# Performance work log

Hardware: AMD Instinct MI355X
Metric: run time of the kernel (lower is better)

The kernel has to match this reference:

```python
import jax, jax.numpy as jnp
import numpy as np

GRID_SIZE = 5
SPLINE_ORDER = 3


def b_splines(x):
    """Cox-de Boor B-spline bases. x: [N, in] -> [N, in, GRID_SIZE+SPLINE_ORDER]."""
    k = SPLINE_ORDER
    h = 2.0 / GRID_SIZE  # grid range [-1, 1]
    grid = jnp.arange(-k, GRID_SIZE + k + 1, dtype=x.dtype) * h - 1.0  # [G+2k+1]
    xe = x[..., None]  # [N, in, 1]
    b = ((xe >= grid[:-1]) & (xe < grid[1:])).astype(x.dtype)
    for j in range(1, k + 1):
        b = ((xe - grid[:-(j + 1)]) / (grid[j:-1] - grid[:-(j + 1)]) * b[..., :-1]
             + (grid[j + 1:] - xe) / (grid[j + 1:] - grid[1:-j]) * b[..., 1:])
    return b  # [N, in, G+k]


def kan_linear(x, base_w, spline_w):
    """efficient-KAN KANLinear: silu base branch + spline branch.
    x: [N, in], base_w: [out, in], spline_w: [out, in, G+k] -> [N, out]."""
    base = jnp.einsum('ni,oi->no', jax.nn.silu(x), base_w)
    spline = jnp.einsum('nig,oig->no', b_splines(x), spline_w)
    return base + spline


def setup_inputs() -> dict:
    key = jax.random.key(0)
    ks = jax.random.split(key, 8)
    C, R, G = 128, 8, GRID_SIZE + SPLINE_ORDER  # in_channels, reduced, n_bases
    B, H, W, D = 2, 64, 64, 64
    s = 0.1  # keep spline weights in a sane init range
    return {
        'x': jax.random.normal(ks[0], (B, C, H, W, D), dtype=jnp.float32),
        'ck1_base': jax.random.normal(ks[1], (R, C), dtype=jnp.float32) * s,
        'ck1_spline': jax.random.normal(ks[2], (R, C, G), dtype=jnp.float32) * s,
        'ck2_base': jax.random.normal(ks[3], (C, R), dtype=jnp.float32) * s,
        'ck2_spline': jax.random.normal(ks[4], (C, R, G), dtype=jnp.float32) * s,
        'conv_w': jax.random.normal(ks[5], (C,), dtype=jnp.float32) * 0.1,
        'sk_base': jax.random.normal(ks[6], (1, 1), dtype=jnp.float32),
        'sk_spline': jax.random.normal(ks[7], (1, 1, G), dtype=jnp.float32),
    }


def reference(x, ck1_base, ck1_spline, ck2_base, ck2_spline, conv_w, sk_base, sk_spline):
    B, C, H, W, D = x.shape
    # channel attention: avg/max pool -> KAN -> ReLU -> KAN, shared weights
    y_avg = jnp.mean(x, axis=(2, 3, 4))  # [B, C]
    y_max = jnp.max(x, axis=(2, 3, 4))   # [B, C]

    def channel_mlp(y):
        h1 = jax.nn.relu(kan_linear(y, ck1_base, ck1_spline))
        return kan_linear(h1, ck2_base, ck2_spline)

    channel_att = jax.nn.sigmoid(channel_mlp(y_avg) + channel_mlp(y_max))
    x_channel = x * channel_att[:, :, None, None, None]

    # spatial attention: 1x1x1 conv (C->1, no bias) then per-voxel 1->1 KAN
    y_spatial = jnp.einsum('bchwd,c->bhwd', x_channel, conv_w)
    y_flat = y_spatial.reshape(-1, 1)  # [B*H*W*D, 1]
    spatial_att = jax.nn.sigmoid(kan_linear(y_flat, sk_base, sk_spline))
    spatial_att = spatial_att.reshape(B, 1, H, W, D)
    return x_channel * spatial_att
```

## Files before the change

### kernel.cpp

```cpp
#include <hip/hip_runtime.h>
#include <math.h>

#define HWD 262144
#define C_CH 128
#define B_N 2
#define VT 128

typedef float f4 __attribute__((ext_vector_type(4)));

__device__ __forceinline__ float sigmoidf_(float v) {
    return 1.0f / (1.0f + expf(-v));
}

__device__ __forceinline__ void bspline8(float x, float* bs) {
    float g[12];
#pragma unroll
    for (int i = 0; i < 12; ++i) g[i] = (float)(i - 3) * 0.4f - 1.0f;
    float b[11];
#pragma unroll
    for (int t = 0; t < 11; ++t) b[t] = (x >= g[t] && x < g[t + 1]) ? 1.0f : 0.0f;
#pragma unroll
    for (int j = 1; j <= 3; ++j) {
#pragma unroll
        for (int t = 0; t + j < 11; ++t) {
            b[t] = (x - g[t]) / (g[t + j] - g[t]) * b[t]
                 + (g[t + j + 1] - x) / (g[t + j + 1] - g[t + 1]) * b[t + 1];
        }
    }
#pragma unroll
    for (int t = 0; t < 8; ++t) bs[t] = b[t];
}

__global__ __launch_bounds__(1024) void k1_pool(const float* __restrict__ x,
                                                float* __restrict__ ws) {
    int bid = blockIdx.x;
    const float4* xp = (const float4*)(x + (size_t)bid * HWD);
    int tid = threadIdx.x;
    float s = 0.0f, m = -INFINITY;
#pragma unroll 4
    for (int i = 0; i < 64; ++i) {
        float4 v = xp[(size_t)i * 1024 + tid];
        s += (v.x + v.y) + (v.z + v.w);
        m = fmaxf(m, fmaxf(fmaxf(v.x, v.y), fmaxf(v.z, v.w)));
    }
#pragma unroll
    for (int off = 32; off > 0; off >>= 1) {
        s += __shfl_xor(s, off, 64);
        m = fmaxf(m, __shfl_xor(m, off, 64));
    }
    __shared__ float ssum[16], smax[16];
    int wave = tid >> 6, lane = tid & 63;
    if (lane == 0) { ssum[wave] = s; smax[wave] = m; }
    __syncthreads();
    if (tid == 0) {
        float S = 0.0f, M = -INFINITY;
#pragma unroll
        for (int w = 0; w < 16; ++w) { S += ssum[w]; M = fmaxf(M, smax[w]); }
        ws[bid]       = S / (float)HWD;
        ws[256 + bid] = M;
    }
}

__global__ __launch_bounds__(512) void k2_catt(const float* ws_in,
                                               const float* __restrict__ ck1_base,
                                               const float* __restrict__ ck1_spline,
                                               const float* __restrict__ ck2_base,
                                               const float* __restrict__ ck2_spline,
                                               const float* __restrict__ conv_w,
                                               float* ws_out) {
    __shared__ float part[512 * 8];
    __shared__ float h1silu[32];
    __shared__ float h1bs[32][8];
    __shared__ float out2[512];
    int t = threadIdx.x;
    {
        int ysel = t >> 8, b = (t >> 7) & 1, i = t & 127;
        float v = ws_in[ysel * 256 + b * 128 + i];
        float sv = v * sigmoidf_(v);
        float bs[8];
        bspline8(v, bs);
#pragma unroll
        for (int r = 0; r < 8; ++r) {
            float acc = sv * ck1_base[r * 128 + i];
#pragma unroll
            for (int g = 0; g < 8; ++g)
                acc += bs[g] * ck1_spline[(r * 128 + i) * 8 + g];
            part[t * 8 + r] = acc;
        }
    }
    __syncthreads();
    if (t < 32) {
        int ysel = t >> 4, b = (t >> 3) & 1, r = t & 7;
        int tb = ysel * 256 + b * 128;
        float acc = 0.0f;
        for (int i = 0; i < 128; ++i) acc += part[(tb + i) * 8 + r];
        float h = fmaxf(acc, 0.0f);
        h1silu[t] = h * sigmoidf_(h);
        bspline8(h, h1bs[t]);
    }
    __syncthreads();
    {
        int ysel = t >> 8, b = (t >> 7) & 1, o = t & 127;
        float acc = 0.0f;
#pragma unroll
        for (int r = 0; r < 8; ++r) {
            int hidx = ysel * 16 + b * 8 + r;
            acc += h1silu[hidx] * ck2_base[o * 8 + r];
#pragma unroll
            for (int g = 0; g < 8; ++g)
                acc += h1bs[hidx][g] * ck2_spline[(o * 8 + r) * 8 + g];
        }
        out2[t] = acc;
    }
    __syncthreads();
    if (t < 256) {
        int o = t & 127;
        float catt = sigmoidf_(out2[t] + out2[256 + t]);
        ws_out[512 + t] = catt;
        ws_out[768 + t] = catt * conv_w[o];
    }
}

__global__ __launch_bounds__(1024) void k3_main(const float* __restrict__ x,
                                                const float* __restrict__ ws,
                                                const float* __restrict__ sk_base,
                                                const float* __restrict__ sk_spline,
                                                float* __restrict__ out) {
    __shared__ __align__(16) float xs[C_CH * VT];
    __shared__ float partial[1024];
    __shared__ __align__(16) float satt[VT];
    __shared__ float catts[C_CH];
    __shared__ float w2s[C_CH];
    int tid = threadIdx.x;
    int bid = blockIdx.x;
    int b = bid >> 11;
    int v0 = (bid & 2047) << 7;
    if (tid < 128) {
        catts[tid] = ws[512 + b * 128 + tid];
        w2s[tid]   = ws[768 + b * 128 + tid];
    }
    const float* xb = x + (size_t)b * C_CH * HWD + v0;
#pragma unroll
    for (int m = 0; m < 4; ++m) {
        int f = m * 1024 + tid;
        int c = f >> 5;
        int j = f & 31;
        f4 v = *(const f4*)(xb + (size_t)c * HWD + j * 4);
        *(f4*)&xs[c * VT + j * 4] = v;
    }
    __syncthreads();
    {
        int v = tid & (VT - 1), q = tid >> 7;
        float acc = 0.0f;
#pragma unroll
        for (int cc = 0; cc < 16; ++cc) {
            int c = q * 16 + cc;
            acc += xs[c * VT + v] * w2s[c];
        }
        partial[tid] = acc;
    }
    __syncthreads();
    if (tid < VT) {
        float s = 0.0f;
#pragma unroll
        for (int k = 0; k < 8; ++k) s += partial[tid + k * 128];
        float bs[8];
        bspline8(s, bs);
        float a = s * sigmoidf_(s) * sk_base[0];
#pragma unroll
        for (int g = 0; g < 8; ++g) a += bs[g] * sk_spline[g];
        satt[tid] = sigmoidf_(a);
    }
    __syncthreads();
    float* ob = out + (size_t)b * C_CH * HWD + v0;
#pragma unroll
    for (int m = 0; m < 4; ++m) {
        int f = m * 1024 + tid;
        int c = f >> 5;
        int j = f & 31;
        f4 v = *(f4*)&xs[c * VT + j * 4];
        f4 sa = *(f4*)&satt[j * 4];
        float ca = catts[c];
        f4 o = v * ca * sa;
        __builtin_nontemporal_store(o, (f4*)(ob + (size_t)c * HWD + j * 4));
    }
}

extern "C" void kernel_launch(void* const* d_in, const int* in_sizes, int n_in,
                              void* d_out, int out_size, void* d_ws, size_t ws_size,
                              hipStream_t stream) {
    const float* x          = (const float*)d_in[0];
    const float* ck1_base   = (const float*)d_in[1];
    const float* ck1_spline = (const float*)d_in[2];
    const float* ck2_base   = (const float*)d_in[3];
    const float* ck2_spline = (const float*)d_in[4];
    const float* conv_w     = (const float*)d_in[5];
    const float* sk_base    = (const float*)d_in[6];
    const float* sk_spline  = (const float*)d_in[7];
    float* out = (float*)d_out;
    float* ws  = (float*)d_ws;

    k1_pool<<<B_N * C_CH, 1024, 0, stream>>>(x, ws);
    k2_catt<<<1, 512, 0, stream>>>(ws, ck1_base, ck1_spline, ck2_base, ck2_spline,
                                   conv_w, ws);
    k3_main<<<B_N * (HWD / VT), 1024, 0, stream>>>(x, ws, sk_base, sk_spline, out);
}
```

Baseline: 493.3 us.

## Fuse channel-attention MLP into persistent main kernel with prefetched double buffer

```diff
diff --git a/kernel.cpp b/kernel.cpp
--- a/kernel.cpp
+++ b/kernel.cpp
@@ -5,6 +5,8 @@
 #define C_CH 128
 #define B_N 2
 #define VT 128
+#define K3_BLOCKS 256
+#define K3_TILES 16
 
 typedef float f4 __attribute__((ext_vector_type(4)));
 
@@ -61,128 +63,154 @@
     }
 }
 
-__global__ __launch_bounds__(512) void k2_catt(const float* ws_in,
-                                               const float* __restrict__ ck1_base,
-                                               const float* __restrict__ ck1_spline,
-                                               const float* __restrict__ ck2_base,
-                                               const float* __restrict__ ck2_spline,
-                                               const float* __restrict__ conv_w,
-                                               float* ws_out) {
-    __shared__ float part[512 * 8];
+__global__ __launch_bounds__(1024) void k3_fused(
+    const float* __restrict__ x, const float* __restrict__ ws,
+    const float* __restrict__ ck1_base, const float* __restrict__ ck1_spline,
+    const float* __restrict__ ck2_base, const float* __restrict__ ck2_spline,
+    const float* __restrict__ conv_w,
+    const float* __restrict__ sk_base, const float* __restrict__ sk_spline,
+    float* __restrict__ out) {
+    __shared__ __align__(16) float xs[2][C_CH * VT];
+    __shared__ float scratch[512 * 8];
+    __shared__ __align__(16) float satt[VT];
+    __shared__ float catts[B_N][C_CH];
+    __shared__ float w2s[B_N][C_CH];
     __shared__ float h1silu[32];
     __shared__ float h1bs[32][8];
     __shared__ float out2[512];
-    int t = threadIdx.x;
+
+    int tid = threadIdx.x;
+    int bid = blockIdx.x;
+
+    f4 rg[4];
     {
-        int ysel = t >> 8, b = (t >> 7) & 1, i = t & 127;
-        float v = ws_in[ysel * 256 + b * 128 + i];
+        const float* xb = x + ((size_t)bid << 7);
+#pragma unroll
+        for (int m = 0; m < 4; ++m) {
+            int f = m * 1024 + tid;
+            int c = f >> 5, j = f & 31;
+            rg[m] = *(const f4*)(xb + (size_t)c * HWD + j * 4);
+        }
+    }
+
+    if (tid < 512) {
+        int pool = tid >> 8, b = (tid >> 7) & 1, i = tid & 127;
+        float v = ws[pool * 256 + b * 128 + i];
         float sv = v * sigmoidf_(v);
-        float bs[8];
-        bspline8(v, bs);
+        float bsv[8];
+        bspline8(v, bsv);
 #pragma unroll
         for (int r = 0; r < 8; ++r) {
             float acc = sv * ck1_base[r * 128 + i];
 #pragma unroll
             for (int g = 0; g < 8; ++g)
-                acc += bs[g] * ck1_spline[(r * 128 + i) * 8 + g];
-            part[t * 8 + r] = acc;
-        }
-    }
-    __syncthreads();
-    if (t < 32) {
-        int ysel = t >> 4, b = (t >> 3) & 1, r = t & 7;
-        int tb = ysel * 256 + b * 128;
+                acc += bsv[g] * ck1_spline[(r * 128 + i) * 8 + g];
+            scratch[tid * 8 + r] = acc;
+        }
+    }
+    __syncthreads();
+    if (tid < 32) {
+        int pool = tid >> 4, b = (tid >> 3) & 1, r = tid & 7;
+        int tb = pool * 256 + b * 128;
         float acc = 0.0f;
-        for (int i = 0; i < 128; ++i) acc += part[(tb + i) * 8 + r];
+        for (int i = 0; i < 128; ++i) acc += scratch[(tb + i) * 8 + r];
         float h = fmaxf(acc, 0.0f);
-        h1silu[t] = h * sigmoidf_(h);
-        bspline8(h, h1bs[t]);
-    }
-    __syncthreads();
-    {
-        int ysel = t >> 8, b = (t >> 7) & 1, o = t & 127;
+        h1silu[tid] = h * sigmoidf_(h);
+        bspline8(h, h1bs[tid]);
+    }
+    __syncthreads();
+    if (tid < 512) {
+        int pool = tid >> 8, b = (tid >> 7) & 1, o = tid & 127;
         float acc = 0.0f;
 #pragma unroll
         for (int r = 0; r < 8; ++r) {
-            int hidx = ysel * 16 + b * 8 + r;
+            int hidx = pool * 16 + b * 8 + r;
             acc += h1silu[hidx] * ck2_base[o * 8 + r];
 #pragma unroll
             for (int g = 0; g < 8; ++g)
                 acc += h1bs[hidx][g] * ck2_spline[(o * 8 + r) * 8 + g];
         }
-        out2[t] = acc;
-    }
-    __syncthreads();
-    if (t < 256) {
-        int o = t & 127;
-        float catt = sigmoidf_(out2[t] + out2[256 + t]);
-        ws_out[512 + t] = catt;
-        ws_out[768 + t] = catt * conv_w[o];
-    }
-}
-
-__global__ __launch_bounds__(1024) void k3_main(const float* __restrict__ x,
-                                                const float* __restrict__ ws,
-                                                const float* __restrict__ sk_base,
-                                                const float* __restrict__ sk_spline,
-                                                float* __restrict__ out) {
-    __shared__ __align__(16) float xs[C_CH * VT];
-    __shared__ float partial[1024];
-    __shared__ __align__(16) float satt[VT];
-    __shared__ float catts[C_CH];
-    __shared__ float w2s[C_CH];
-    int tid = threadIdx.x;
-    int bid = blockIdx.x;
-    int b = bid >> 11;
-    int v0 = (bid & 2047) << 7;
-    if (tid < 128) {
-        catts[tid] = ws[512 + b * 128 + tid];
-        w2s[tid]   = ws[768 + b * 128 + tid];
-    }
-    const float* xb = x + (size_t)b * C_CH * HWD + v0;
+        out2[tid] = acc;
+    }
+    __syncthreads();
+    if (tid < 256) {
+        int b = tid >> 7, o = tid & 127;
+        float catt = sigmoidf_(out2[b * 128 + o] + out2[256 + b * 128 + o]);
+        catts[b][o] = catt;
+        w2s[b][o]   = catt * conv_w[o];
+    }
 #pragma unroll
     for (int m = 0; m < 4; ++m) {
         int f = m * 1024 + tid;
-        int c = f >> 5;
-        int j = f & 31;
-        f4 v = *(const f4*)(xb + (size_t)c * HWD + j * 4);
-        *(f4*)&xs[c * VT + j * 4] = v;
-    }
-    __syncthreads();
-    {
-        int v = tid & (VT - 1), q = tid >> 7;
-        float acc = 0.0f;
-#pragma unroll
-        for (int cc = 0; cc < 16; ++cc) {
-            int c = q * 16 + cc;
-            acc += xs[c * VT + v] * w2s[c];
-        }
-        partial[tid] = acc;
-    }
-    __syncthreads();
-    if (tid < VT) {
-        float s = 0.0f;
-#pragma unroll
-        for (int k = 0; k < 8; ++k) s += partial[tid + k * 128];
-        float bs[8];
-        bspline8(s, bs);
-        float a = s * sigmoidf_(s) * sk_base[0];
-#pragma unroll
-        for (int g = 0; g < 8; ++g) a += bs[g] * sk_spline[g];
-        satt[tid] = sigmoidf_(a);
-    }
-    __syncthreads();
-    float* ob = out + (size_t)b * C_CH * HWD + v0;
-#pragma unroll
-    for (int m = 0; m < 4; ++m) {
-        int f = m * 1024 + tid;
-        int c = f >> 5;
-        int j = f & 31;
-        f4 v = *(f4*)&xs[c * VT + j * 4];
-        f4 sa = *(f4*)&satt[j * 4];
-        float ca = catts[c];
-        f4 o = v * ca * sa;
-        __builtin_nontemporal_store(o, (f4*)(ob + (size_t)c * HWD + j * 4));
+        int c = f >> 5, j = f & 31;
+        *(f4*)&xs[0][c * VT + j * 4] = rg[m];
+    }
+    __syncthreads();
+
+    int buf = 0;
+    for (int it = 0; it < K3_TILES; ++it) {
+        int b  = it >> 3;
+        int v0 = (((it & 7) << 8) + bid) << 7;
+        float* ob = out + (size_t)b * C_CH * HWD + v0;
+
+        f4 rn[4];
+        int itn = it + 1;
+        if (itn < K3_TILES) {
+            int bn  = itn >> 3;
+            int v0n = (((itn & 7) << 8) + bid) << 7;
+            const float* xbn = x + (size_t)bn * C_CH * HWD + v0n;
+#pragma unroll
+            for (int m = 0; m < 4; ++m) {
+                int f = m * 1024 + tid;
+                int c = f >> 5, j = f & 31;
+                rn[m] = *(const f4*)(xbn + (size_t)c * HWD + j * 4);
+            }
+        }
+
+        {
+            int v = tid & (VT - 1), q = tid >> 7;
+            float acc = 0.0f;
+#pragma unroll
+            for (int cc = 0; cc < 16; ++cc) {
+                int c = q * 16 + cc;
+                acc += xs[buf][c * VT + v] * w2s[b][c];
+            }
+            scratch[tid] = acc;
+        }
+        __syncthreads();
+        if (tid < VT) {
+            float s = 0.0f;
+#pragma unroll
+            for (int k = 0; k < 8; ++k) s += scratch[tid + k * 128];
+            float bs[8];
+            bspline8(s, bs);
+            float a = s * sigmoidf_(s) * sk_base[0];
+#pragma unroll
+            for (int g = 0; g < 8; ++g) a += bs[g] * sk_spline[g];
+            satt[tid] = sigmoidf_(a);
+        }
+        __syncthreads();
+#pragma unroll
+        for (int m = 0; m < 4; ++m) {
+            int f = m * 1024 + tid;
+            int c = f >> 5, j = f & 31;
+            f4 vv = *(f4*)&xs[buf][c * VT + j * 4];
+            f4 sa = *(f4*)&satt[j * 4];
+            float ca = catts[b][c];
+            f4 o = vv * ca * sa;
+            __builtin_nontemporal_store(o, (f4*)(ob + (size_t)c * HWD + j * 4));
+        }
+        if (itn < K3_TILES) {
+            int nb = buf ^ 1;
+#pragma unroll
+            for (int m = 0; m < 4; ++m) {
+                int f = m * 1024 + tid;
+                int c = f >> 5, j = f & 31;
+                *(f4*)&xs[nb][c * VT + j * 4] = rn[m];
+            }
+            buf = nb;
+        }
+        __syncthreads();
     }
 }
 
@@ -201,7 +229,7 @@
     float* ws  = (float*)d_ws;
 
     k1_pool<<<B_N * C_CH, 1024, 0, stream>>>(x, ws);
-    k2_catt<<<1, 512, 0, stream>>>(ws, ck1_base, ck1_spline, ck2_base, ck2_spline,
-                                   conv_w, ws);
-    k3_main<<<B_N * (HWD / VT), 1024, 0, stream>>>(x, ws, sk_base, sk_spline, out);
-}
+    k3_fused<<<K3_BLOCKS, 1024, 0, stream>>>(x, ws, ck1_base, ck1_spline,
+                                             ck2_base, ck2_spline, conv_w,
+                                             sk_base, sk_spline, out);
+}
```

After: 492.8 us. Within noise of the previous version (-0.1%).
